# Kernel optimization log

Hardware: AMD Instinct MI355X
Metric: run time of the kernel (lower is better)

The kernel has to match this reference:

```python
import jax, jax.numpy as jnp
import numpy as np

N_NODES = 50000
N_EDGES = 800000
IN_DIM = 128
OUT_DIM = 128
N_REL = 8


def setup_inputs() -> dict:
    key = jax.random.key(0)
    k1, k2, k3, k4, k5 = jax.random.split(key, 5)
    x = jax.random.normal(k1, (N_NODES, IN_DIM), dtype=jnp.float32)
    edge_index = jax.random.randint(k2, (2, N_EDGES), 0, N_NODES, dtype=jnp.int32).astype(jnp.int64)
    edge_type = jax.random.randint(k3, (N_EDGES,), 0, N_REL, dtype=jnp.int32).astype(jnp.int64)
    W = jax.random.normal(k4, (N_REL, IN_DIM, OUT_DIM), dtype=jnp.float32) * 0.02
    W0 = jax.random.normal(k5, (IN_DIM, OUT_DIM), dtype=jnp.float32) * 0.02
    return {"x": x, "edge_index": edge_index, "edge_type": edge_type,
            "num_nodes": N_NODES, "W": W, "W0": W0}


def reference(x, edge_index, edge_type, num_nodes, W, W0):
    src = edge_index[0]
    dst = edge_index[1]
    # Per-relation transform of ALL nodes, matching the original loop's x @ W[r].
    xW = jnp.einsum('nd,rdo->rno', x, W)            # [R, N, OUT]
    msgs = xW[edge_type, src]                       # [E, OUT] gather per edge
    agg = jax.ops.segment_sum(msgs, dst, num_segments=num_nodes)  # scatter-add to dst
    out = x @ W0 + agg                              # root/self term
    deg = jax.ops.segment_sum(jnp.ones_like(dst, dtype=out.dtype), dst,
                              num_segments=num_nodes)
    deg = jnp.maximum(deg, 1.0)
    return out / deg[:, None]
```

## Files before the change

### kernel.cpp

```cpp
#include <hip/hip_runtime.h>
#include <hip/hip_bf16.h>
#include <cstdint>
#include <cstddef>


#define NDIM 128
#define NREL 8
#define KR   1024
#define KCAT 1152
#define COARSE 196
#define EPB 4096

typedef __attribute__((ext_vector_type(8))) short bf16x8;
typedef __attribute__((ext_vector_type(4))) float f32x4;
typedef unsigned int uint32;

__device__ __forceinline__ short f2bf(float f){
  __hip_bfloat16 h = __float2bfloat16(f);
  return *reinterpret_cast<short*>(&h);
}
__device__ __forceinline__ float bfl(uint32 v){ return __uint_as_float(v << 16); }
__device__ __forceinline__ float bfh(uint32 v){ return __uint_as_float(v & 0xFFFF0000u); }

__device__ __forceinline__ void gload_lds16(const void* g, void* l){
  __builtin_amdgcn_global_load_lds(
      (const __attribute__((address_space(1))) unsigned int*)g,
      (__attribute__((address_space(3))) unsigned int*)l, 16, 0, 0);
}

__global__ void k_prep(const float* __restrict__ x, uint32* __restrict__ xb, int n4, int xblocks,
                       const float* __restrict__ W, const float* __restrict__ W0,
                       short* __restrict__ Wb, int wblocks,
                       const int* __restrict__ ei, int* flag, int* coarse_cnt){
  int b = blockIdx.x;
  if (b < xblocks){
    int i = b * 256 + threadIdx.x;
    if (i >= n4) return;
    float4 f = ((const float4*)x)[i];
    uint32 lo = ((uint32)(unsigned short)f2bf(f.x)) | (((uint32)(unsigned short)f2bf(f.y)) << 16);
    uint32 hi = ((uint32)(unsigned short)f2bf(f.z)) | (((uint32)(unsigned short)f2bf(f.w)) << 16);
    ((uint2*)xb)[i] = make_uint2(lo, hi);
  } else if (b < xblocks + wblocks){
    int i = (b - xblocks) * 256 + threadIdx.x;
    if (i >= NDIM * KCAT) return;
    int j  = i / KCAT;
    int t  = i - j * KCAT;
    int r  = t >> 7;
    int kd = t & 127;
    float v = (r < NREL) ? W[(((size_t)r * NDIM + kd) << 7) + j] : W0[((size_t)kd << 7) + j];
    Wb[i] = f2bf(v);
  } else {
    if (threadIdx.x < COARSE) coarse_cnt[threadIdx.x] = 0;
    if (threadIdx.x < 64){
      int v = ei[2 * threadIdx.x + 1];
      unsigned long long m = __ballot(v == 0);
      if (threadIdx.x == 0) flag[0] = (m == ~0ull) ? 1 : 0;
    }
  }
}

__global__ __launch_bounds__(1024) void k_hist(
    const int* __restrict__ ei, const int* __restrict__ et, const int* __restrict__ flag,
    uint32* __restrict__ kv, unsigned char* __restrict__ ctmp,
    int* __restrict__ coarse_cnt, int* __restrict__ blockRes, int E){
  __shared__ int h[COARSE];
  const int b = blockIdx.x;
  for (int i = threadIdx.x; i < COARSE; i += 1024) h[i] = 0;
  __syncthreads();
  const int is64 = flag[0];
  const int e0 = b * EPB;
  for (int i = threadIdx.x; i < EPB; i += 1024){
    int e = e0 + i;
    if (e < E){
      int s, d, t;
      if (is64){ s = ei[2*e]; d = ei[2*(E + e)]; t = et[2*e]; }
      else     { s = ei[e];   d = ei[E + e];     t = et[e];   }
      int c = d >> 8;
      kv[e]   = (uint32)s | ((uint32)t << 16) | ((uint32)(d & 255) << 19);
      ctmp[e] = (unsigned char)c;
      atomicAdd(&h[c], 1);
    }
  }
  __syncthreads();
  for (int c = threadIdx.x; c < COARSE; c += 1024){
    int cnt = h[c];
    int res = 0;
    if (cnt > 0) res = atomicAdd(&coarse_cnt[c], cnt);
    blockRes[b * COARSE + c] = res;
  }
}

__global__ void k_base(const int* __restrict__ coarse_cnt, int* __restrict__ base){
  __shared__ int sm[256];
  int t = threadIdx.x;
  int v = (t < COARSE) ? coarse_cnt[t] : 0;
  sm[t] = v; __syncthreads();
  #pragma unroll
  for (int off = 1; off < 256; off <<= 1){
    int xv = 0; if (t >= off) xv = sm[t - off];
    __syncthreads(); sm[t] += xv; __syncthreads();
  }
  if (t <= COARSE) base[t] = sm[t] - v;
}

__global__ __launch_bounds__(1024) void k_cscatter(
    const uint32* __restrict__ kv, const unsigned char* __restrict__ ctmp,
    const int* __restrict__ base, const int* __restrict__ blockRes,
    uint32* __restrict__ ckv, int E){
  __shared__ int cur[COARSE];
  const int b = blockIdx.x;
  for (int c = threadIdx.x; c < COARSE; c += 1024)
    cur[c] = base[c] + blockRes[b * COARSE + c];
  __syncthreads();
  const int e0 = b * EPB;
  for (int i = threadIdx.x; i < EPB; i += 1024){
    int e = e0 + i;
    if (e < E){
      uint32 v = kv[e];
      int c = ctmp[e];
      int pos = atomicAdd(&cur[c], 1);
      ckv[pos] = v;
    }
  }
}

__global__ __launch_bounds__(1024) void k_fine(
    const uint32* __restrict__ ckv, const int* __restrict__ base,
    uint32* __restrict__ esort, int* __restrict__ rs, int N){
  __shared__ int h[256];
  __shared__ int cur[256];
  const int c  = blockIdx.x;
  const int lo = base[c], hi = base[c + 1];
  const int t  = threadIdx.x;
  if (t < 256) h[t] = 0;
  __syncthreads();
  for (int i = lo + t; i < hi; i += 1024)
    atomicAdd(&h[(ckv[i] >> 19) & 255], 1);
  __syncthreads();
  int v = (t < 256) ? h[t] : 0;
  __syncthreads();
  for (int off = 1; off < 256; off <<= 1){
    int xv = 0;
    if (t < 256 && t >= off) xv = h[t - off];
    __syncthreads();
    if (t < 256) h[t] += xv;
    __syncthreads();
  }
  if (t < 256){
    int excl = h[t] - v;
    cur[t] = lo + excl;
    int idx = c * 256 + t;
    if (idx <= N) rs[idx] = lo + excl;
  }
  __syncthreads();
  for (int i = lo + t; i < hi; i += 1024){
    uint32 v2 = ckv[i];
    int pos = atomicAdd(&cur[(v2 >> 19) & 255], 1);
    esort[pos] = v2;
  }
}

#define ACCUM(P, V) \
  switch (((P) >> 16) & 7){ \
    case 0: acc[0].x+=bfl(V); acc[0].y+=bfh(V); break; case 1: acc[1].x+=bfl(V); acc[1].y+=bfh(V); break; \
    case 2: acc[2].x+=bfl(V); acc[2].y+=bfh(V); break; case 3: acc[3].x+=bfl(V); acc[3].y+=bfh(V); break; \
    case 4: acc[4].x+=bfl(V); acc[4].y+=bfh(V); break; case 5: acc[5].x+=bfl(V); acc[5].y+=bfh(V); break; \
    case 6: acc[6].x+=bfl(V); acc[6].y+=bfh(V); break; case 7: acc[7].x+=bfl(V); acc[7].y+=bfh(V); break; \
  }

__global__ __launch_bounds__(256) void k_agg(const uint32* __restrict__ xb,
                                             const int* __restrict__ rs,
                                             const uint32* __restrict__ esort,
                                             uint32* __restrict__ hcat,
                                             float* __restrict__ invdeg, int N){
  int wave = threadIdx.x >> 6;
  int lane = threadIdx.x & 63;
  int n = blockIdx.x * 4 + wave;
  if (n >= N) return;
  int beg = rs[n], end = rs[n + 1];
  float2 acc[NREL];
  #pragma unroll
  for (int r = 0; r < NREL; ++r){ acc[r].x = 0.f; acc[r].y = 0.f; }

  int i = beg;
  for (; i + 7 < end; i += 8){
    uint32 p0 = esort[i],   p1 = esort[i+1], p2 = esort[i+2], p3 = esort[i+3];
    uint32 p4 = esort[i+4], p5 = esort[i+5], p6 = esort[i+6], p7 = esort[i+7];
    uint32 v0 = xb[(size_t)(p0 & 0xFFFF) * 64 + lane];
    uint32 v1 = xb[(size_t)(p1 & 0xFFFF) * 64 + lane];
    uint32 v2 = xb[(size_t)(p2 & 0xFFFF) * 64 + lane];
    uint32 v3 = xb[(size_t)(p3 & 0xFFFF) * 64 + lane];
    uint32 v4 = xb[(size_t)(p4 & 0xFFFF) * 64 + lane];
    uint32 v5 = xb[(size_t)(p5 & 0xFFFF) * 64 + lane];
    uint32 v6 = xb[(size_t)(p6 & 0xFFFF) * 64 + lane];
    uint32 v7 = xb[(size_t)(p7 & 0xFFFF) * 64 + lane];
    ACCUM(p0, v0) ACCUM(p1, v1) ACCUM(p2, v2) ACCUM(p3, v3)
    ACCUM(p4, v4) ACCUM(p5, v5) ACCUM(p6, v6) ACCUM(p7, v7)
  }
  for (; i + 3 < end; i += 4){
    uint32 p0 = esort[i], p1 = esort[i+1], p2 = esort[i+2], p3 = esort[i+3];
    uint32 v0 = xb[(size_t)(p0 & 0xFFFF) * 64 + lane];
    uint32 v1 = xb[(size_t)(p1 & 0xFFFF) * 64 + lane];
    uint32 v2 = xb[(size_t)(p2 & 0xFFFF) * 64 + lane];
    uint32 v3 = xb[(size_t)(p3 & 0xFFFF) * 64 + lane];
    ACCUM(p0, v0) ACCUM(p1, v1) ACCUM(p2, v2) ACCUM(p3, v3)
  }
  for (; i < end; ++i){
    uint32 p = esort[i];
    uint32 v = xb[(size_t)(p & 0xFFFF) * 64 + lane];
    ACCUM(p, v)
  }

  size_t b2 = (size_t)n * (KR / 2);
  #pragma unroll
  for (int r = 0; r < NREL; ++r){
    __hip_bfloat162 pk = __float22bfloat162_rn(make_float2(acc[r].x, acc[r].y));
    __builtin_nontemporal_store(*reinterpret_cast<uint32*>(&pk), &hcat[b2 + r * 64 + lane]);
  }
  if (lane == 0){
    int d = end - beg;
    invdeg[n] = 1.0f / (float)(d > 0 ? d : 1);
  }
}

__global__ __launch_bounds__(512) void k_gemm2(
    const short* __restrict__ acat,
    const short* __restrict__ xbs,
    const short* __restrict__ wb,
    const float* __restrict__ invdeg,
    float* __restrict__ out, int N)
{
  __shared__ char smem[65536];
  char* As0 = smem;
  char* As1 = smem + 16384;
  char* Bs0 = smem + 32768;
  char* Bs1 = smem + 49152;

  const int tid  = threadIdx.x;
  const int lane = tid & 63;
  const int wid  = tid >> 6;
  const int wr   = wid >> 1;
  const int wc   = wid & 1;
  const int n0   = blockIdx.x * 128;
  const int lr   = lane & 15;
  const int lq   = lane >> 4;

  f32x4 acc[2][4];
  #pragma unroll
  for (int m = 0; m < 2; ++m)
    #pragma unroll
    for (int p = 0; p < 4; ++p)
      acc[m][p] = (f32x4){0.f, 0.f, 0.f, 0.f};

  const int srow = tid >> 3;
  const int scs  = tid & 7;

  auto STAGE = [&](char* Ab, char* Bb, int ks){
    const short* ab;
    size_t rstride;
    if (ks < 16){ ab = acat + (size_t)n0 * KR + ks * 64;          rstride = KR;  }
    else        { ab = xbs  + (size_t)n0 * 128 + (ks - 16) * 64;  rstride = 128; }
    #pragma unroll
    for (int q = 0; q < 2; ++q){
      int row = q * 64 + srow;
      const short* src = ab + (size_t)row * rstride + ((scs ^ (row & 7)) << 3);
      gload_lds16(src, Ab + q * 8192 + (wid << 10));
    }
    const short* bb = wb + ks * 64;
    #pragma unroll
    for (int q = 0; q < 2; ++q){
      int j = q * 64 + srow;
      const short* src = bb + (size_t)j * KCAT + ((scs ^ (j & 7)) << 3);
      gload_lds16(src, Bb + q * 8192 + (wid << 10));
    }
  };

  auto COMPUTE = [&](const char* Ab, const char* Bb){
    bf16x8 a[2][2], b[2][4];
    #pragma unroll
    for (int kk = 0; kk < 2; ++kk){
      #pragma unroll
      for (int m = 0; m < 2; ++m){
        int row = wr * 32 + m * 16 + lr;
        int c   = kk * 4 + lq;
        a[kk][m] = *(const bf16x8*)(Ab + row * 128 + ((c ^ (row & 7)) << 4));
      }
      #pragma unroll
      for (int p = 0; p < 4; ++p){
        int j = wc * 64 + p * 16 + lr;
        int c = kk * 4 + lq;
        b[kk][p] = *(const bf16x8*)(Bb + j * 128 + ((c ^ (j & 7)) << 4));
      }
    }
    #pragma unroll
    for (int kk = 0; kk < 2; ++kk)
      #pragma unroll
      for (int m = 0; m < 2; ++m)
        #pragma unroll
        for (int p = 0; p < 4; ++p)
          acc[m][p] = __builtin_amdgcn_mfma_f32_16x16x32_bf16(a[kk][m], b[kk][p], acc[m][p], 0, 0, 0);
  };

  STAGE(As0, Bs0, 0);
  __syncthreads();
  for (int ks = 0; ks < 18; ks += 2){
    STAGE(As1, Bs1, ks + 1);
    COMPUTE(As0, Bs0);
    __syncthreads();
    if (ks + 2 < 18) STAGE(As0, Bs0, ks + 2);
    COMPUTE(As1, Bs1);
    __syncthreads();
  }

  #pragma unroll
  for (int m = 0; m < 2; ++m){
    int rbase = n0 + wr * 32 + m * 16 + lq * 4;
    #pragma unroll
    for (int v = 0; v < 4; ++v){
      int ro = rbase + v;
      if (ro < N){
        float inv = invdeg[ro];
        #pragma unroll
        for (int p = 0; p < 4; ++p)
          __builtin_nontemporal_store(acc[m][p][v] * inv,
              &out[(((size_t)ro) << 7) + wc * 64 + p * 16 + lr]);
      }
    }
  }
}

extern "C" void kernel_launch(void* const* d_in, const int* in_sizes, int n_in,
                              void* d_out, int out_size, void* d_ws, size_t ws_size,
                              hipStream_t stream){
  const float* x  = (const float*)d_in[0];
  const int*   ei = (const int*)d_in[1];
  const int*   et = (const int*)d_in[2];
  const float* W  = (const float*)d_in[4];
  const float* W0 = (const float*)d_in[5];
  float* out = (float*)d_out;

  const int N = in_sizes[0] / NDIM;
  const int E = in_sizes[2];
  const int Npad = N + 128;
  const int nblkE = (E + EPB - 1) / EPB;

  char* ws = (char*)d_ws;
  size_t off = 0;
  auto alloc = [&](size_t bytes)->size_t{
    size_t p = off; off = (off + bytes + 255) & ~(size_t)255; return p;
  };
  size_t o_flag = alloc(4);
  size_t o_kv   = alloc((size_t)E * 4);
  size_t o_ct   = alloc((size_t)E);
  size_t o_ckv  = alloc((size_t)E * 4);
  size_t o_es   = alloc((size_t)E * 4);
  size_t o_cc   = alloc(COARSE * 4);
  size_t o_base = alloc((COARSE + 2) * 4);
  size_t o_br   = alloc((size_t)nblkE * COARSE * 4);
  size_t o_rs   = alloc((size_t)(N + 1) * 4);
  size_t o_inv  = alloc((size_t)N * 4);
  size_t o_h    = alloc((size_t)Npad * KR * 2);
  size_t o_wb   = alloc((size_t)NDIM * KCAT * 2);
  size_t o_xb   = alloc((size_t)Npad * NDIM * 2);
  (void)ws_size;

  int*  flag   = (int*)(ws + o_flag);
  uint32* kv   = (uint32*)(ws + o_kv);
  unsigned char* ctmp = (unsigned char*)(ws + o_ct);
  uint32* ckv  = (uint32*)(ws + o_ckv);
  uint32* esort= (uint32*)(ws + o_es);
  int*  ccnt   = (int*)(ws + o_cc);
  int*  base   = (int*)(ws + o_base);
  int*  bres   = (int*)(ws + o_br);
  int*  rs     = (int*)(ws + o_rs);
  float* invdeg= (float*)(ws + o_inv);
  uint32* hcat = (uint32*)(ws + o_h);
  short* acat  = (short*)(ws + o_h);
  short* Wbs   = (short*)(ws + o_wb);
  uint32* xb   = (uint32*)(ws + o_xb);
  short* xbs   = (short*)(ws + o_xb);

  const int n4      = N * NDIM / 4;
  const int xblocks = (n4 + 255) / 256;
  const int wblocks = (NDIM * KCAT + 255) / 256;

  k_prep<<<xblocks + wblocks + 1, 256, 0, stream>>>(
      x, xb, n4, xblocks, W, W0, Wbs, wblocks, ei, flag, ccnt);
  k_hist<<<nblkE, 1024, 0, stream>>>(ei, et, flag, kv, ctmp, ccnt, bres, E);
  k_base<<<1, 256, 0, stream>>>(ccnt, base);
  k_cscatter<<<nblkE, 1024, 0, stream>>>(kv, ctmp, base, bres, ckv, E);
  k_fine<<<COARSE, 1024, 0, stream>>>(ckv, base, esort, rs, N);
  k_agg<<<(N + 3) / 4, 256, 0, stream>>>(xb, rs, esort, hcat, invdeg, N);
  k_gemm2<<<(N + 127) / 128, 512, 0, stream>>>(acat, xbs, Wbs, invdeg, out, N);
}
```

Measured before the change: 105.3 us.

## Sort edges by relation within each destination and stream per-relation accumulation

The fine bucketing pass now keys on destination node plus relation type (2048 bins per block, scanned with a 1024-thread prefix sum), so edges reach each node grouped by relation. The aggregation kernel then keeps a single running accumulator and flushes it to the relation's slot whenever the relation changes, writing zeros for relations with no edges. This replaces the 8-way switch over eight accumulator pairs and cuts register pressure and branching. Edge-list loads become nontemporal. The price is a larger shared histogram and scan in the sort, plus data-dependent flush branches inside the loop.

```diff
diff --git a/kernel.cpp b/kernel.cpp
--- a/kernel.cpp
+++ b/kernel.cpp
@@ -127,46 +127,38 @@
 __global__ __launch_bounds__(1024) void k_fine(
     const uint32* __restrict__ ckv, const int* __restrict__ base,
     uint32* __restrict__ esort, int* __restrict__ rs, int N){
-  __shared__ int h[256];
-  __shared__ int cur[256];
+  __shared__ int h[2048];
+  __shared__ int part[1024];
+  __shared__ int cur[2048];
   const int c  = blockIdx.x;
   const int lo = base[c], hi = base[c + 1];
   const int t  = threadIdx.x;
-  if (t < 256) h[t] = 0;
+  h[2*t] = 0; h[2*t + 1] = 0;
   __syncthreads();
   for (int i = lo + t; i < hi; i += 1024)
-    atomicAdd(&h[(ckv[i] >> 19) & 255], 1);
-  __syncthreads();
-  int v = (t < 256) ? h[t] : 0;
-  __syncthreads();
-  for (int off = 1; off < 256; off <<= 1){
-    int xv = 0;
-    if (t < 256 && t >= off) xv = h[t - off];
-    __syncthreads();
-    if (t < 256) h[t] += xv;
-    __syncthreads();
-  }
-  if (t < 256){
-    int excl = h[t] - v;
-    cur[t] = lo + excl;
-    int idx = c * 256 + t;
+    atomicAdd(&h[(ckv[i] >> 16) & 0x7FF], 1);
+  __syncthreads();
+  int v0 = h[2*t], v1 = h[2*t + 1];
+  int s = v0 + v1;
+  part[t] = s; __syncthreads();
+  for (int off = 1; off < 1024; off <<= 1){
+    int xv = 0; if (t >= off) xv = part[t - off];
+    __syncthreads(); part[t] += xv; __syncthreads();
+  }
+  int excl = part[t] - s;
+  cur[2*t]     = lo + excl;
+  cur[2*t + 1] = lo + excl + v0;
+  if ((t & 3) == 0){
+    int idx = c * 256 + (t >> 2);
     if (idx <= N) rs[idx] = lo + excl;
   }
   __syncthreads();
   for (int i = lo + t; i < hi; i += 1024){
     uint32 v2 = ckv[i];
-    int pos = atomicAdd(&cur[(v2 >> 19) & 255], 1);
+    int pos = atomicAdd(&cur[(v2 >> 16) & 0x7FF], 1);
     esort[pos] = v2;
   }
 }
-
-#define ACCUM(P, V) \
-  switch (((P) >> 16) & 7){ \
-    case 0: acc[0].x+=bfl(V); acc[0].y+=bfh(V); break; case 1: acc[1].x+=bfl(V); acc[1].y+=bfh(V); break; \
-    case 2: acc[2].x+=bfl(V); acc[2].y+=bfh(V); break; case 3: acc[3].x+=bfl(V); acc[3].y+=bfh(V); break; \
-    case 4: acc[4].x+=bfl(V); acc[4].y+=bfh(V); break; case 5: acc[5].x+=bfl(V); acc[5].y+=bfh(V); break; \
-    case 6: acc[6].x+=bfl(V); acc[6].y+=bfh(V); break; case 7: acc[7].x+=bfl(V); acc[7].y+=bfh(V); break; \
-  }
 
 __global__ __launch_bounds__(256) void k_agg(const uint32* __restrict__ xb,
                                              const int* __restrict__ rs,
@@ -178,14 +170,35 @@
   int n = blockIdx.x * 4 + wave;
   if (n >= N) return;
   int beg = rs[n], end = rs[n + 1];
-  float2 acc[NREL];
-  #pragma unroll
-  for (int r = 0; r < NREL; ++r){ acc[r].x = 0.f; acc[r].y = 0.f; }
+  size_t b2 = (size_t)n * (KR / 2);
+
+  float ax = 0.f, ay = 0.f;
+  int cur_r = 0;
+
+  auto FLUSH = [&](int upto){
+    __hip_bfloat162 pk = __float22bfloat162_rn(make_float2(ax, ay));
+    __builtin_nontemporal_store(*reinterpret_cast<uint32*>(&pk),
+                                &hcat[b2 + cur_r * 64 + lane]);
+    for (int r = cur_r + 1; r < upto; ++r)
+      __builtin_nontemporal_store(0u, &hcat[b2 + r * 64 + lane]);
+    ax = 0.f; ay = 0.f;
+    cur_r = upto;
+  };
+
+  #define PROC(P, V) { int tt = (int)(((P) >> 16) & 7); \
+                       if (tt != cur_r) FLUSH(tt); \
+                       ax += bfl(V); ay += bfh(V); }
 
   int i = beg;
   for (; i + 7 < end; i += 8){
-    uint32 p0 = esort[i],   p1 = esort[i+1], p2 = esort[i+2], p3 = esort[i+3];
-    uint32 p4 = esort[i+4], p5 = esort[i+5], p6 = esort[i+6], p7 = esort[i+7];
+    uint32 p0 = __builtin_nontemporal_load(&esort[i]);
+    uint32 p1 = __builtin_nontemporal_load(&esort[i+1]);
+    uint32 p2 = __builtin_nontemporal_load(&esort[i+2]);
+    uint32 p3 = __builtin_nontemporal_load(&esort[i+3]);
+    uint32 p4 = __builtin_nontemporal_load(&esort[i+4]);
+    uint32 p5 = __builtin_nontemporal_load(&esort[i+5]);
+    uint32 p6 = __builtin_nontemporal_load(&esort[i+6]);
+    uint32 p7 = __builtin_nontemporal_load(&esort[i+7]);
     uint32 v0 = xb[(size_t)(p0 & 0xFFFF) * 64 + lane];
     uint32 v1 = xb[(size_t)(p1 & 0xFFFF) * 64 + lane];
     uint32 v2 = xb[(size_t)(p2 & 0xFFFF) * 64 + lane];
@@ -194,29 +207,28 @@
     uint32 v5 = xb[(size_t)(p5 & 0xFFFF) * 64 + lane];
     uint32 v6 = xb[(size_t)(p6 & 0xFFFF) * 64 + lane];
     uint32 v7 = xb[(size_t)(p7 & 0xFFFF) * 64 + lane];
-    ACCUM(p0, v0) ACCUM(p1, v1) ACCUM(p2, v2) ACCUM(p3, v3)
-    ACCUM(p4, v4) ACCUM(p5, v5) ACCUM(p6, v6) ACCUM(p7, v7)
+    PROC(p0, v0) PROC(p1, v1) PROC(p2, v2) PROC(p3, v3)
+    PROC(p4, v4) PROC(p5, v5) PROC(p6, v6) PROC(p7, v7)
   }
   for (; i + 3 < end; i += 4){
-    uint32 p0 = esort[i], p1 = esort[i+1], p2 = esort[i+2], p3 = esort[i+3];
+    uint32 p0 = __builtin_nontemporal_load(&esort[i]);
+    uint32 p1 = __builtin_nontemporal_load(&esort[i+1]);
+    uint32 p2 = __builtin_nontemporal_load(&esort[i+2]);
+    uint32 p3 = __builtin_nontemporal_load(&esort[i+3]);
     uint32 v0 = xb[(size_t)(p0 & 0xFFFF) * 64 + lane];
     uint32 v1 = xb[(size_t)(p1 & 0xFFFF) * 64 + lane];
     uint32 v2 = xb[(size_t)(p2 & 0xFFFF) * 64 + lane];
     uint32 v3 = xb[(size_t)(p3 & 0xFFFF) * 64 + lane];
-    ACCUM(p0, v0) ACCUM(p1, v1) ACCUM(p2, v2) ACCUM(p3, v3)
+    PROC(p0, v0) PROC(p1, v1) PROC(p2, v2) PROC(p3, v3)
   }
   for (; i < end; ++i){
-    uint32 p = esort[i];
+    uint32 p = __builtin_nontemporal_load(&esort[i]);
     uint32 v = xb[(size_t)(p & 0xFFFF) * 64 + lane];
-    ACCUM(p, v)
-  }
-
-  size_t b2 = (size_t)n * (KR / 2);
-  #pragma unroll
-  for (int r = 0; r < NREL; ++r){
-    __hip_bfloat162 pk = __float22bfloat162_rn(make_float2(acc[r].x, acc[r].y));
-    __builtin_nontemporal_store(*reinterpret_cast<uint32*>(&pk), &hcat[b2 + r * 64 + lane]);
-  }
+    PROC(p, v)
+  }
+  FLUSH(NREL);
+  #undef PROC
+
   if (lane == 0){
     int d = end - beg;
     invdeg[n] = 1.0f / (float)(d > 0 ? d : 1);
```

After: 123.9 us. 17.7% more time.
